# Performance work log

Measured on AMD Instinct MI355X. Metric: run time of the kernel, lower is better.

## Reference

```python
import jax, jax.numpy as jnp
import numpy as np

D_MODEL = 1024
EXPANSION = 4
NUM_TILES = 4
D_FF = D_MODEL * EXPANSION


def setup_inputs() -> dict:
    key = jax.random.key(0)
    k1, k2, k3, k4, k5 = jax.random.split(key, 5)
    x = jax.random.normal(k1, (8, 2048, D_MODEL), dtype=jnp.float32)
    w_up = jax.random.normal(k2, (D_FF, D_MODEL), dtype=jnp.float32) * 0.02
    b_up = jax.random.normal(k3, (D_FF,), dtype=jnp.float32) * 0.02
    w_down = jax.random.normal(k4, (D_MODEL, D_FF), dtype=jnp.float32) * 0.02
    b_down = jax.random.normal(k5, (D_MODEL,), dtype=jnp.float32) * 0.02
    return {"x": x, "w_up": w_up, "b_up": b_up, "w_down": w_down, "b_down": b_down}


def reference(x, w_up, b_up, w_down, b_down):
    B, T, C = x.shape
    xf = x.reshape(B * T, C)  # [N, d_model]
    N = B * T

    # Emergent tile signatures: sign of per-tile row sums of up_proj weight.
    tile_up = D_FF // NUM_TILES
    signatures = jnp.sign(w_up.reshape(NUM_TILES, tile_up, C).sum(axis=1))  # [num_tiles, d_model]

    # Routing: argmax over input-signature alignment -> one-hot gate.
    scores = xf @ signatures.T                      # [N, num_tiles]
    winner = jnp.argmax(scores, axis=-1)            # [N]
    gate = jax.nn.one_hot(winner, NUM_TILES, dtype=xf.dtype)  # [N, num_tiles]

    # Tile-gated up projection (gate scales output tile blocks), then ReLU.
    hidden = xf @ w_up.T + b_up                     # [N, d_ff]
    hidden = (hidden.reshape(N, NUM_TILES, tile_up) * gate[:, :, None]).reshape(N, D_FF)
    hidden = jax.nn.relu(hidden)

    # Tile-gated down projection.
    tile_down = D_MODEL // NUM_TILES
    out = hidden @ w_down.T + b_down                # [N, d_model]
    out = (out.reshape(N, NUM_TILES, tile_down) * gate[:, :, None]).reshape(N, D_MODEL)

    return out.reshape(B, T, D_MODEL), gate.reshape(B, T, NUM_TILES)
```

## Files before the change

### kernel.cpp

```cpp
#include <hip/hip_runtime.h>
#include <stdint.h>
#include <stddef.h>

#define N_TOK 16384
#define DM    1024
#define DFF   4096
#define NT    4
#define TU    1024
#define TD    256

typedef __attribute__((ext_vector_type(8))) short  short8;
typedef __attribute__((ext_vector_type(4))) short  short4v;
typedef __attribute__((ext_vector_type(4))) float  floatx4;

__device__ inline unsigned short f2bf(float f){
  union { float f; uint32_t u; } v; v.f = f;
  uint32_t u = v.u + 0x7FFFu + ((v.u >> 16) & 1u);
  return (unsigned short)(u >> 16);
}

__device__ __forceinline__ void gll16(const void* g, void* l){
  __builtin_amdgcn_global_load_lds(
      (const __attribute__((address_space(1))) unsigned int*)g,
      (__attribute__((address_space(3))) unsigned int*)l,
      16, 0, 0);
}

__global__ void k_prep(const float* __restrict__ w_up,
                       float* __restrict__ partial,
                       unsigned short* __restrict__ wupb){
  const int tid = threadIdx.x;
  const int b = blockIdx.x;
  const int tile = b >> 6, chunk = b & 63;
  const int c0 = tid * 4;
  const int row0 = tile*TU + chunk*16;
  float s0=0.f, s1=0.f, s2=0.f, s3=0.f;
  const float* base = w_up + (size_t)row0 * DM + c0;
  #pragma unroll
  for (int r = 0; r < 16; ++r){
    floatx4 v = *(const floatx4*)(base + (size_t)r * DM);
    s0 += v[0]; s1 += v[1]; s2 += v[2]; s3 += v[3];
    short4v p;
    p[0]=(short)f2bf(v[0]); p[1]=(short)f2bf(v[1]);
    p[2]=(short)f2bf(v[2]); p[3]=(short)f2bf(v[3]);
    *(short4v*)(wupb + (size_t)(row0 + r) * DM + c0) = p;
  }
  float* p = partial + ((size_t)tile*DM + c0) * 64 + chunk;
  p[0] = s0; p[64] = s1; p[128] = s2; p[192] = s3;
}

__global__ void k_sig_final(const float* __restrict__ partial,
                            float* __restrict__ sig){
  const int g = blockIdx.x * 256 + threadIdx.x;
  const float* p = partial + (size_t)g * 64;
  float s = 0.f;
  #pragma unroll
  for (int i = 0; i < 64; ++i) s += p[i];
  sig[g] = (s > 0.f) ? 1.f : ((s < 0.f) ? -1.f : 0.f);
}

__global__ __launch_bounds__(256) void k_route(
    const float* __restrict__ x, const float* __restrict__ sig,
    const float* __restrict__ w_down, unsigned short* __restrict__ wdownb,
    float* __restrict__ gate_out, int* __restrict__ winner,
    unsigned short* __restrict__ xbf){
  const int tid = threadIdx.x;
  if (blockIdx.x >= 1024){
    const size_t i = ((size_t)(blockIdx.x - 1024) * 256 + tid) * 8;
    floatx4 v0 = *(const floatx4*)(w_down + i);
    floatx4 v1 = *(const floatx4*)(w_down + i + 4);
    short8 p;
    p[0]=(short)f2bf(v0[0]); p[1]=(short)f2bf(v0[1]); p[2]=(short)f2bf(v0[2]); p[3]=(short)f2bf(v0[3]);
    p[4]=(short)f2bf(v1[0]); p[5]=(short)f2bf(v1[1]); p[6]=(short)f2bf(v1[2]); p[7]=(short)f2bf(v1[3]);
    *(short8*)(wdownb + i) = p;
    return;
  }
  __shared__ float ssig[NT * DM];
  for (int i = tid; i < NT*DM; i += 256) ssig[i] = sig[i];
  __syncthreads();
  const int wv = tid >> 6, lane = tid & 63;

  floatx4 sg[4][4];
  #pragma unroll
  for (int j = 0; j < 4; ++j){
    const int c = j*256 + lane*4;
    #pragma unroll
    for (int tt = 0; tt < 4; ++tt)
      sg[j][tt] = *(const floatx4*)(ssig + tt*DM + c);
  }

  #pragma unroll
  for (int t = 0; t < 4; ++t){
    const int n = blockIdx.x * 16 + wv * 4 + t;
    const float* xr = x + (size_t)n * DM;
    unsigned short* xb = xbf + (size_t)n * 2048 + 1024;
    double a0=0.0, a1=0.0, a2=0.0, a3=0.0;
    #pragma unroll
    for (int j = 0; j < 4; ++j){
      const int c = j*256 + lane*4;
      floatx4 v = *(const floatx4*)(xr + c);
      short4v p;
      p[0]=(short)f2bf(v[0]); p[1]=(short)f2bf(v[1]);
      p[2]=(short)f2bf(v[2]); p[3]=(short)f2bf(v[3]);
      *(short4v*)(xb + c) = p;
      #pragma unroll
      for (int u = 0; u < 4; ++u){
        double xv = (double)v[u];
        a0 += xv * (double)sg[j][0][u];
        a1 += xv * (double)sg[j][1][u];
        a2 += xv * (double)sg[j][2][u];
        a3 += xv * (double)sg[j][3][u];
      }
    }
    #pragma unroll
    for (int off = 32; off > 0; off >>= 1){
      a0 += __shfl_down(a0, off, 64);
      a1 += __shfl_down(a1, off, 64);
      a2 += __shfl_down(a2, off, 64);
      a3 += __shfl_down(a3, off, 64);
    }
    if (lane == 0){
      double s[4] = {a0, a1, a2, a3};
      int w = 0;
      #pragma unroll
      for (int tt = 1; tt < 4; ++tt) if (s[tt] > s[w]) w = tt;
      floatx4 g = { w==0 ? 1.f:0.f, w==1 ? 1.f:0.f, w==2 ? 1.f:0.f, w==3 ? 1.f:0.f };
      *(floatx4*)(gate_out + (size_t)n * 4) = g;
      winner[n] = w;
    }
  }
}

__global__ void k_hist(const int* __restrict__ winner,
                       int* __restrict__ blk_cnt){
  __shared__ int wcnt[4][NT];
  const int tid = threadIdx.x, wv = tid >> 6, lane = tid & 63;
  const int w = winner[blockIdx.x * 256 + tid];
  #pragma unroll
  for (int t = 0; t < NT; ++t){
    unsigned long long m = __ballot(w == t);
    if (lane == 0) wcnt[wv][t] = __popcll(m);
  }
  __syncthreads();
  if (tid < NT){
    int s = wcnt[0][tid] + wcnt[1][tid] + wcnt[2][tid] + wcnt[3][tid];
    blk_cnt[blockIdx.x * NT + tid] = s;
  }
}

__global__ void k_scan(const int* __restrict__ blk_cnt,
                       int* __restrict__ meta, int* __restrict__ blk_base){
  __shared__ int s[256];
  const int tid = threadIdx.x;
  s[tid] = blk_cnt[tid];
  __syncthreads();
  if (tid == 0){
    int tot[NT] = {0,0,0,0};
    for (int b = 0; b < 64; ++b)
      for (int t = 0; t < NT; ++t) tot[t] += s[b*NT + t];
    int off = 0, base[NT];
    for (int t = 0; t < NT; ++t){ meta[t] = tot[t]; meta[4+t] = off; base[t] = off; off += tot[t]; }
    for (int b = 0; b < 64; ++b)
      for (int t = 0; t < NT; ++t){ int c = s[b*NT + t]; s[b*NT + t] = base[t]; base[t] += c; }
  }
  __syncthreads();
  blk_base[tid] = s[tid];
}

__global__ void k_scatter(const int* __restrict__ winner,
                          const int* __restrict__ blk_base,
                          int* __restrict__ idx){
  __shared__ int wcnt[4][NT];
  const int tid = threadIdx.x, wv = tid >> 6, lane = tid & 63;
  const int n = blockIdx.x * 256 + tid;
  const int w = winner[n];
  unsigned long long mymask = 0;
  #pragma unroll
  for (int t = 0; t < NT; ++t){
    unsigned long long m = __ballot(w == t);
    if (lane == 0) wcnt[wv][t] = __popcll(m);
    if (t == w) mymask = m;
  }
  __syncthreads();
  const unsigned long long below = (lane == 0) ? 0ull : (~0ull >> (64 - lane));
  int pos = blk_base[blockIdx.x * NT + w] + __popcll(mymask & below);
  for (int v = 0; v < wv; ++v) pos += wcnt[v][w];
  idx[pos] = n;
}

__global__ __launch_bounds__(256, 2) void k_gemm1(
    const unsigned short* __restrict__ xbf,
    const unsigned short* __restrict__ wupb,
    const float* __restrict__ b_up, const int* __restrict__ meta,
    const int* __restrict__ idx, unsigned short* __restrict__ hid){
  const int lin  = blockIdx.x;
  const int r    = lin & 7, q = lin >> 3;
  const int tile = r >> 1;
  const int nb   = q & 7;
  const int chunk = ((q >> 3) << 1) | (r & 1);
  const int p0   = chunk * 128;

  const int cnt  = meta[tile];
  if (p0 >= cnt) return;
  const int off  = meta[4 + tile];

  __shared__ unsigned short smem[16384];
  unsigned short* As0 = smem;
  unsigned short* As1 = smem + 4096;
  unsigned short* Bs0 = smem + 8192;
  unsigned short* Bs1 = smem + 12288;

  const int tid = threadIdx.x;
  const int wv = tid >> 6, lane = tid & 63;
  const int wm = (wv >> 1) * 64, wn = (wv & 1) * 64;
  const int l16 = lane & 15, quad = lane >> 4;
  const int rsub = lane >> 2;
  const int kus  = (lane & 3) * 8;

  int* nrs = (int*)smem;
  if (tid < 128){
    int p = p0 + tid;
    nrs[tid] = idx[off + (p < cnt ? p : cnt - 1)];
  }
  __syncthreads();
  const int ra = wv*32 + rsub;
  const unsigned short* aptr0 = xbf + (size_t)nrs[ra]      * 2048 + 1024 + kus;
  const unsigned short* aptr1 = xbf + (size_t)nrs[ra + 16] * 2048 + 1024 + kus;
  int  enr[2][4];
  bool ev [2][4];
  #pragma unroll
  for (int half = 0; half < 2; ++half){
    #pragma unroll
    for (int s = 0; s < 4; ++s){
      const int lrow = (tid + s*256) >> 4;
      const int m = half*64 + lrow;
      ev [half][s] = (p0 + m < cnt);
      enr[half][s] = nrs[m];
    }
  }
  __syncthreads();

  const unsigned short* bptr0 = wupb + (size_t)(tile*TU + nb*128 + wv*32 + rsub) * DM + kus;
  const unsigned short* bptr1 = bptr0 + 16 * DM;

  unsigned short* a0d0 = As0 + (wv*32) * 32;  unsigned short* a0d1 = a0d0 + 16*32;
  unsigned short* a1d0 = As1 + (wv*32) * 32;  unsigned short* a1d1 = a1d0 + 16*32;
  unsigned short* b0d0 = Bs0 + (wv*32) * 32;  unsigned short* b0d1 = b0d0 + 16*32;
  unsigned short* b1d0 = Bs1 + (wv*32) * 32;  unsigned short* b1d1 = b1d0 + 16*32;

  floatx4 acc[4][4];
  #pragma unroll
  for (int i = 0; i < 4; ++i)
    #pragma unroll
    for (int j = 0; j < 4; ++j) acc[i][j] = (floatx4){0.f,0.f,0.f,0.f};

  for (int k0 = 0; k0 < DM; k0 += 64){
    gll16(aptr0 + k0,      a0d0);
    gll16(aptr1 + k0,      a0d1);
    gll16(aptr0 + k0 + 32, a1d0);
    gll16(aptr1 + k0 + 32, a1d1);
    gll16(bptr0 + k0,      b0d0);
    gll16(bptr1 + k0,      b0d1);
    gll16(bptr0 + k0 + 32, b1d0);
    gll16(bptr1 + k0 + 32, b1d1);
    __syncthreads();
    {
      short8 af[4], bfr[4];
      #pragma unroll
      for (int i = 0; i < 4; ++i) af[i]  = *(const short8*)(As0 + (wm + i*16 + l16)*32 + quad*8);
      #pragma unroll
      for (int j = 0; j < 4; ++j) bfr[j] = *(const short8*)(Bs0 + (wn + j*16 + l16)*32 + quad*8);
      #pragma unroll
      for (int i = 0; i < 4; ++i)
        #pragma unroll
        for (int j = 0; j < 4; ++j)
          acc[i][j] = __builtin_amdgcn_mfma_f32_16x16x32_bf16(af[i], bfr[j], acc[i][j], 0, 0, 0);
    }
    {
      short8 af[4], bfr[4];
      #pragma unroll
      for (int i = 0; i < 4; ++i) af[i]  = *(const short8*)(As1 + (wm + i*16 + l16)*32 + quad*8);
      #pragma unroll
      for (int j = 0; j < 4; ++j) bfr[j] = *(const short8*)(Bs1 + (wn + j*16 + l16)*32 + quad*8);
      #pragma unroll
      for (int i = 0; i < 4; ++i)
        #pragma unroll
        for (int j = 0; j < 4; ++j)
          acc[i][j] = __builtin_amdgcn_mfma_f32_16x16x32_bf16(af[i], bfr[j], acc[i][j], 0, 0, 0);
    }
    __syncthreads();
  }

  const int gcol0 = nb*128;
  #pragma unroll
  for (int half = 0; half < 2; ++half){
    if ((wv >> 1) == half){
      #pragma unroll
      for (int i = 0; i < 4; ++i){
        #pragma unroll
        for (int j = 0; j < 4; ++j){
          const int col = wn + j*16 + l16;
          const float bias = b_up[tile*TU + gcol0 + col];
          #pragma unroll
          for (int r2 = 0; r2 < 4; ++r2){
            const int lrow = i*16 + quad*4 + r2;
            float v = acc[i][j][r2] + bias;
            smem[lrow*136 + col] = f2bf(v > 0.f ? v : 0.f);
          }
        }
      }
    }
    __syncthreads();
    #pragma unroll
    for (int s = 0; s < 4; ++s){
      const int c = tid + s*256;
      const int lrow = c >> 4, k8 = (c & 15) * 8;
      if (ev[half][s]){
        short8 vv = *(const short8*)(smem + lrow*136 + k8);
        *(short8*)(hid + (size_t)enr[half][s]*2048 + gcol0 + k8) = vv;
      }
    }
    __syncthreads();
  }
}

__global__ __launch_bounds__(256, 2) void k_gemm2(
    const unsigned short* __restrict__ hid,
    const unsigned short* __restrict__ wdownb,
    const float* __restrict__ b_down, const int* __restrict__ meta,
    const int* __restrict__ idx, float* __restrict__ out){
  const int lin  = blockIdx.x;
  const int r    = lin & 7, q = lin >> 3;
  const int tile = r >> 1;
  const int xx   = (q << 1) | (r & 1);
  const int p0   = xx * 32;

  const int cnt  = meta[tile];
  if (p0 >= cnt) return;
  const int off  = meta[4 + tile];

  __shared__ unsigned short smem[18432];
  unsigned short* As0 = smem;
  unsigned short* As1 = smem + 1024;
  unsigned short* Bs0 = smem + 2048;
  unsigned short* Bs1 = smem + 10240;
  float* epi = (float*)smem;
  __shared__ int nrow[32];

  const int tid = threadIdx.x;
  if (tid < 32){
    int p = p0 + tid;
    nrow[tid] = idx[off + (p < cnt ? p : cnt - 1)];
  }
  __syncthreads();

  const int wv = tid >> 6, lane = tid & 63;
  const int wn = wv * 64;
  const int l16 = lane & 15, quad = lane >> 4;

  const int rsub = lane >> 2;
  const int kus  = (lane & 3) * 8;

  const int arow = (wv & 1)*16 + rsub;
  const unsigned short* aptr = hid + (size_t)nrow[arow] * 2048 + kus;
  const int aoff = (wv >> 1) * 32;
  unsigned short* asd = (wv < 2 ? As0 : As1) + ((wv & 1)*16) * 32;
  const unsigned short* bptr = wdownb + (size_t)(tile*TD + wv*64 + rsub) * DFF + tile*TU + kus;
  unsigned short* bsd0 = Bs0 + (wv*64) * 32;
  unsigned short* bsd1 = Bs1 + (wv*64) * 32;

  floatx4 acc[2][4];
  #pragma unroll
  for (int i = 0; i < 2; ++i)
    #pragma unroll
    for (int j = 0; j < 4; ++j) acc[i][j] = (floatx4){0.f,0.f,0.f,0.f};

  for (int k0 = 0; k0 < TU; k0 += 64){
    gll16(aptr + k0 + aoff, asd);
    gll16(bptr + k0,               bsd0);
    gll16(bptr + k0 + 16*DFF,      bsd0 + 16*32);
    gll16(bptr + k0 + 32*DFF,      bsd0 + 32*32);
    gll16(bptr + k0 + 48*DFF,      bsd0 + 48*32);
    gll16(bptr + k0 + 32,          bsd1);
    gll16(bptr + k0 + 32 + 16*DFF, bsd1 + 16*32);
    gll16(bptr + k0 + 32 + 32*DFF, bsd1 + 32*32);
    gll16(bptr + k0 + 32 + 48*DFF, bsd1 + 48*32);
    __syncthreads();
    {
      short8 af[2], bfr[4];
      #pragma unroll
      for (int i = 0; i < 2; ++i) af[i]  = *(const short8*)(As0 + (i*16 + l16)*32 + quad*8);
      #pragma unroll
      for (int j = 0; j < 4; ++j) bfr[j] = *(const short8*)(Bs0 + (wn + j*16 + l16)*32 + quad*8);
      #pragma unroll
      for (int i = 0; i < 2; ++i)
        #pragma unroll
        for (int j = 0; j < 4; ++j)
          acc[i][j] = __builtin_amdgcn_mfma_f32_16x16x32_bf16(af[i], bfr[j], acc[i][j], 0, 0, 0);
    }
    {
      short8 af[2], bfr[4];
      #pragma unroll
      for (int i = 0; i < 2; ++i) af[i]  = *(const short8*)(As1 + (i*16 + l16)*32 + quad*8);
      #pragma unroll
      for (int j = 0; j < 4; ++j) bfr[j] = *(const short8*)(Bs1 + (wn + j*16 + l16)*32 + quad*8);
      #pragma unroll
      for (int i = 0; i < 2; ++i)
        #pragma unroll
        for (int j = 0; j < 4; ++j)
          acc[i][j] = __builtin_amdgcn_mfma_f32_16x16x32_bf16(af[i], bfr[j], acc[i][j], 0, 0, 0);
    }
    __syncthreads();
  }

  const floatx4 z4 = {0.f, 0.f, 0.f, 0.f};
  #pragma unroll
  for (int cb = 0; cb < 4; ++cb){
    if (cb == tile) continue;
    for (int c = tid; c < 32*64; c += 256){
      const int rowl = c >> 6, c4 = (c & 63) * 4;
      if (p0 + rowl < cnt)
        *(floatx4*)(out + (size_t)nrow[rowl]*DM + cb*256 + c4) = z4;
    }
  }

  #pragma unroll
  for (int half = 0; half < 2; ++half){
    #pragma unroll
    for (int j = 0; j < 4; ++j){
      const int col = wn + j*16 + l16;
      const float bias = b_down[tile*TD + col];
      #pragma unroll
      for (int r2 = 0; r2 < 4; ++r2){
        const int lrow = quad*4 + r2;
        epi[lrow*260 + col] = acc[half][j][r2] + bias;
      }
    }
    __syncthreads();
    #pragma unroll
    for (int c = tid; c < 1024; c += 256){
      const int lrow = c >> 6, c4 = (c & 63) * 4;
      const int m = half*16 + lrow;
      if (p0 + m < cnt){
        floatx4 v = *(const floatx4*)(epi + lrow*260 + c4);
        *(floatx4*)(out + (size_t)nrow[m]*DM + tile*TD + c4) = v;
      }
    }
    __syncthreads();
  }
}

extern "C" void kernel_launch(void* const* d_in, const int* in_sizes, int n_in,
                              void* d_out, int out_size, void* d_ws, size_t ws_size,
                              hipStream_t stream){
  const float* x      = (const float*)d_in[0];
  const float* w_up   = (const float*)d_in[1];
  const float* b_up   = (const float*)d_in[2];
  const float* w_down = (const float*)d_in[3];
  const float* b_down = (const float*)d_in[4];

  unsigned short* wupb   = (unsigned short*)d_ws;
  unsigned short* wdownb = wupb + (size_t)DFF * DM;
  float* partial = (float*)(wdownb + (size_t)DM * DFF);
  float* sig     = partial + 262144;
  int*   ints    = (int*)(sig + 4096);
  int*   winner   = ints;
  int*   idx      = ints + 16384;
  int*   meta     = ints + 32768;
  int*   blk_cnt  = ints + 32776;
  int*   blk_base = ints + 33032;

  float*          out  = (float*)d_out;
  float*          gate = out + (size_t)N_TOK * DM;
  unsigned short* ob16 = (unsigned short*)d_out;

  k_prep      <<<dim3(256),  256, 0, stream>>>(w_up, partial, wupb);
  k_sig_final <<<dim3(16),   256, 0, stream>>>(partial, sig);
  k_route     <<<dim3(3072), 256, 0, stream>>>(x, sig, w_down, wdownb, gate, winner, ob16);
  k_hist      <<<dim3(64),   256, 0, stream>>>(winner, blk_cnt);
  k_scan      <<<dim3(1),    256, 0, stream>>>(blk_cnt, meta, blk_base);
  k_scatter   <<<dim3(64),   256, 0, stream>>>(winner, blk_base, idx);
  k_gemm1     <<<dim3(4096), 256, 0, stream>>>(ob16, wupb, b_up, meta, idx, ob16);
  k_gemm2     <<<dim3(2048), 256, 0, stream>>>(ob16, wdownb, b_down, meta, idx, out);
}
```

Measured before the change: 257.0 us.

## Double-buffer LDS in down-projection GEMM with prefetch two stages ahead

```diff
diff --git a/kernel.cpp b/kernel.cpp
--- a/kernel.cpp
+++ b/kernel.cpp
@@ -339,11 +339,7 @@
   if (p0 >= cnt) return;
   const int off  = meta[4 + tile];
 
-  __shared__ unsigned short smem[18432];
-  unsigned short* As0 = smem;
-  unsigned short* As1 = smem + 1024;
-  unsigned short* Bs0 = smem + 2048;
-  unsigned short* Bs1 = smem + 10240;
+  __shared__ unsigned short smem[36864];
   float* epi = (float*)smem;
   __shared__ int nrow[32];
 
@@ -357,17 +353,16 @@
   const int wv = tid >> 6, lane = tid & 63;
   const int wn = wv * 64;
   const int l16 = lane & 15, quad = lane >> 4;
-
   const int rsub = lane >> 2;
   const int kus  = (lane & 3) * 8;
 
   const int arow = (wv & 1)*16 + rsub;
   const unsigned short* aptr = hid + (size_t)nrow[arow] * 2048 + kus;
   const int aoff = (wv >> 1) * 32;
-  unsigned short* asd = (wv < 2 ? As0 : As1) + ((wv & 1)*16) * 32;
+  const int asdo = (wv < 2 ? 0 : 1024) + ((wv & 1)*16) * 32;
   const unsigned short* bptr = wdownb + (size_t)(tile*TD + wv*64 + rsub) * DFF + tile*TU + kus;
-  unsigned short* bsd0 = Bs0 + (wv*64) * 32;
-  unsigned short* bsd1 = Bs1 + (wv*64) * 32;
+  const int bsd0o = 2048  + (wv*64) * 32;
+  const int bsd1o = 10240 + (wv*64) * 32;
 
   floatx4 acc[2][4];
   #pragma unroll
@@ -375,23 +370,28 @@
     #pragma unroll
     for (int j = 0; j < 4; ++j) acc[i][j] = (floatx4){0.f,0.f,0.f,0.f};
 
-  for (int k0 = 0; k0 < TU; k0 += 64){
-    gll16(aptr + k0 + aoff, asd);
-    gll16(bptr + k0,               bsd0);
-    gll16(bptr + k0 + 16*DFF,      bsd0 + 16*32);
-    gll16(bptr + k0 + 32*DFF,      bsd0 + 32*32);
-    gll16(bptr + k0 + 48*DFF,      bsd0 + 48*32);
-    gll16(bptr + k0 + 32,          bsd1);
-    gll16(bptr + k0 + 32 + 16*DFF, bsd1 + 16*32);
-    gll16(bptr + k0 + 32 + 32*DFF, bsd1 + 32*32);
-    gll16(bptr + k0 + 32 + 48*DFF, bsd1 + 48*32);
-    __syncthreads();
+  auto stage = [&](int buf, int s){
+    unsigned short* base = smem + buf*18432;
+    const int k0 = s*64;
+    gll16(aptr + k0 + aoff,        base + asdo);
+    gll16(bptr + k0,               base + bsd0o);
+    gll16(bptr + k0 + 16*DFF,      base + bsd0o + 512);
+    gll16(bptr + k0 + 32*DFF,      base + bsd0o + 1024);
+    gll16(bptr + k0 + 48*DFF,      base + bsd0o + 1536);
+    gll16(bptr + k0 + 32,          base + bsd1o);
+    gll16(bptr + k0 + 32 + 16*DFF, base + bsd1o + 512);
+    gll16(bptr + k0 + 32 + 32*DFF, base + bsd1o + 1024);
+    gll16(bptr + k0 + 32 + 48*DFF, base + bsd1o + 1536);
+  };
+
+  auto compute = [&](int buf){
+    const unsigned short* base = smem + buf*18432;
     {
       short8 af[2], bfr[4];
       #pragma unroll
-      for (int i = 0; i < 2; ++i) af[i]  = *(const short8*)(As0 + (i*16 + l16)*32 + quad*8);
-      #pragma unroll
-      for (int j = 0; j < 4; ++j) bfr[j] = *(const short8*)(Bs0 + (wn + j*16 + l16)*32 + quad*8);
+      for (int i = 0; i < 2; ++i) af[i]  = *(const short8*)(base + (i*16 + l16)*32 + quad*8);
+      #pragma unroll
+      for (int j = 0; j < 4; ++j) bfr[j] = *(const short8*)(base + 2048 + (wn + j*16 + l16)*32 + quad*8);
       #pragma unroll
       for (int i = 0; i < 2; ++i)
         #pragma unroll
@@ -401,16 +401,30 @@
     {
       short8 af[2], bfr[4];
       #pragma unroll
-      for (int i = 0; i < 2; ++i) af[i]  = *(const short8*)(As1 + (i*16 + l16)*32 + quad*8);
-      #pragma unroll
-      for (int j = 0; j < 4; ++j) bfr[j] = *(const short8*)(Bs1 + (wn + j*16 + l16)*32 + quad*8);
+      for (int i = 0; i < 2; ++i) af[i]  = *(const short8*)(base + 1024 + (i*16 + l16)*32 + quad*8);
+      #pragma unroll
+      for (int j = 0; j < 4; ++j) bfr[j] = *(const short8*)(base + 10240 + (wn + j*16 + l16)*32 + quad*8);
       #pragma unroll
       for (int i = 0; i < 2; ++i)
         #pragma unroll
         for (int j = 0; j < 4; ++j)
           acc[i][j] = __builtin_amdgcn_mfma_f32_16x16x32_bf16(af[i], bfr[j], acc[i][j], 0, 0, 0);
     }
-    __syncthreads();
+  };
+
+  stage(0, 0);
+  stage(1, 1);
+
+  for (int s = 0; s < 16; ++s){
+    if (s == 15) asm volatile("s_waitcnt vmcnt(0)" ::: "memory");
+    else         asm volatile("s_waitcnt vmcnt(9)" ::: "memory");
+    __builtin_amdgcn_s_barrier();
+    __builtin_amdgcn_sched_barrier(0);
+    compute(s & 1);
+    __builtin_amdgcn_sched_barrier(0);
+    asm volatile("" ::: "memory");
+    __builtin_amdgcn_s_barrier();
+    if (s < 14) stage(s & 1, s + 2);
   }
 
   const floatx4 z4 = {0.f, 0.f, 0.f, 0.f};
```

Result: no change. 260.0 us (+1.2%).
